# Optimization experiments

Hardware: AMD Instinct MI355X
Metric: run time of the kernel (lower is better)

The kernel has to match this reference:

```python
import jax, jax.numpy as jnp
import numpy as np

B, T, DIM, H = 4, 2048, 1024, 16
NOPE, ROPE, VDIM, KVR = 128, 64, 128, 512
QKD = NOPE + ROPE  # 192
SCALE = QKD ** -0.5
THETA = 10000.0


def apply_rope(x, cos, sin):
    # x: (B, T, H, D) with interleaved (real, imag) pairs; cos/sin: (T, D//2)
    xr, xi = x[..., 0::2], x[..., 1::2]
    c = cos[None, :, None, :]
    s = sin[None, :, None, :]
    yr = xr * c - xi * s
    yi = xr * s + xi * c
    return jnp.stack([yr, yi], axis=-1).reshape(x.shape)


def rms_norm(x, eps=1e-6):
    return x * jax.lax.rsqrt(jnp.mean(x * x, axis=-1, keepdims=True) + eps)


def setup_inputs() -> dict:
    key = jax.random.key(0)
    ks = jax.random.split(key, 10)
    def lin(k, fan_in, fan_out):
        bound = 1.0 / np.sqrt(fan_in)
        kw, kb = jax.random.split(k)
        w = jax.random.uniform(kw, (fan_out, fan_in), jnp.float32, -bound, bound)
        b = jax.random.uniform(kb, (fan_out,), jnp.float32, -bound, bound)
        return w, b
    wq_w, wq_b = lin(ks[0], DIM, H * QKD)
    wkv_a_w, wkv_a_b = lin(ks[1], DIM, KVR + ROPE)
    wkv_b_w, wkv_b_b = lin(ks[2], KVR, H * (NOPE + VDIM))
    wo_w, wo_b = lin(ks[3], H * VDIM, DIM)
    x = jax.random.normal(ks[4], (B, T, DIM), jnp.float32)
    inv_freq = THETA ** (-jnp.arange(0, ROPE, 2, dtype=jnp.float32) / ROPE)  # (32,)
    ang = jnp.arange(T, dtype=jnp.float32)[:, None] * inv_freq[None, :]  # (T, 32)
    return {
        "x": x,
        "wq_w": wq_w, "wq_b": wq_b,
        "wkv_a_w": wkv_a_w, "wkv_a_b": wkv_a_b,
        "wkv_b_w": wkv_b_w, "wkv_b_b": wkv_b_b,
        "wo_w": wo_w, "wo_b": wo_b,
        "freqs_cos": jnp.cos(ang), "freqs_sin": jnp.sin(ang),
        "start_pos": 0,
    }


def reference(x, wq_w, wq_b, wkv_a_w, wkv_a_b, wkv_b_w, wkv_b_b, wo_w, wo_b,
              freqs_cos, freqs_sin, start_pos):
    b, t, _ = x.shape
    # Q projection, split into nope + rope parts
    q = (x @ wq_w.T + wq_b).reshape(b, t, H, QKD)
    q_nope, q_rope = q[..., :NOPE], q[..., NOPE:]
    q_rope = apply_rope(q_rope, freqs_cos, freqs_sin)
    q = jnp.concatenate([q_nope, q_rope], axis=-1)  # (B,T,H,192)
    # low-rank KV latent + shared rope key
    kv_a = x @ wkv_a_w.T + wkv_a_b  # (B,T,576)
    kv_lat, k_rope = kv_a[..., :KVR], kv_a[..., KVR:]
    k_rope = apply_rope(k_rope[:, :, None, :], freqs_cos, freqs_sin)  # (B,T,1,64)
    # decompress latent -> k_nope, v
    kv = (rms_norm(kv_lat) @ wkv_b_w.T + wkv_b_b).reshape(b, t, H, NOPE + VDIM)
    k_nope, v = kv[..., :NOPE], kv[..., NOPE:]
    k = jnp.concatenate([k_nope, jnp.broadcast_to(k_rope, (b, t, H, ROPE))], axis=-1)
    # causal SDPA (start_pos=0 prefill: cache[:end_pos] == current k/v)
    scores = jnp.einsum("bthd,bshd->bhts", q, k) * SCALE
    causal = jnp.tril(jnp.ones((t, t), dtype=bool))
    scores = jnp.where(causal[None, None], scores, jnp.finfo(scores.dtype).min)
    probs = jax.nn.softmax(scores, axis=-1)
    out = jnp.einsum("bhts,bshd->bthd", probs, v).reshape(b, t, H * VDIM)
    return out @ wo_w.T + wo_b
```

## Files before the change

### kernel.cpp

```cpp
#include <hip/hip_runtime.h>
#include <hip/hip_bf16.h>
#include <cmath>

#define B_    4
#define T_    2048
#define DIM_  1024
#define H_    16
#define NOPE_ 128
#define ROPE_ 64
#define VDIM_ 128
#define KVR_  512
#define QKD_  192
#define NTOK  (B_ * T_)

static constexpr float SCALE2_ = 0.07216878364870322f * 1.4426950408889634f;

typedef __attribute__((ext_vector_type(8))) unsigned short ushort8_t;
typedef __bf16 v8bf __attribute__((ext_vector_type(8)));
typedef float  v4f  __attribute__((ext_vector_type(4)));

__device__ __forceinline__ float bf2f(unsigned short u) {
    return __uint_as_float(((unsigned int)u) << 16);
}
__device__ __forceinline__ unsigned short f2bf(float f) {
    unsigned int u = __float_as_uint(f);
    u += 0x7FFFu + ((u >> 16) & 1u);
    return (unsigned short)(u >> 16);
}
__device__ __forceinline__ unsigned short f2bf_hw(float f) {
    return __builtin_bit_cast(unsigned short, (__bf16)f);
}
__device__ __forceinline__ void store1(float* p, float v)          { *p = v; }
__device__ __forceinline__ void store1(__hip_bfloat16* p, float v) { *p = __float2bfloat16(v); }

__device__ __forceinline__ float exp2_hw(float x) {
    return __builtin_amdgcn_exp2f(x);
}

__device__ __forceinline__ void load_lds16(const void* g, void* l) {
    __builtin_amdgcn_global_load_lds(
        (const __attribute__((address_space(1))) void*)g,
        (__attribute__((address_space(3))) void*)l, 16, 0, 0);
}

__device__ __forceinline__ void cvt4(const float* s, __hip_bfloat16* d, int q4) {
    const int i = q4 * 4;
    const float4 v = *(const float4*)(s + i);
    ushort4 o;
    o.x = f2bf(v.x); o.y = f2bf(v.y); o.z = f2bf(v.z); o.w = f2bf(v.w);
    *(ushort4*)((unsigned short*)d + i) = o;
}

#define X4_   (NTOK*1024/4)
#define Q4_   (3072*1024/4)
#define KB4_  (4096*512/4)
#define O4_   (1024*2048/4)
#define A4_   (640*1024/4)
#define CVT_TOTAL (X4_ + Q4_ + KB4_ + O4_ + A4_)

__global__ __launch_bounds__(256) void cvt_all(
    const float* __restrict__ x,    const float* __restrict__ wq,
    const float* __restrict__ wkvb, const float* __restrict__ wo,
    const float* __restrict__ wkva, const float* __restrict__ wkva_bias,
    __hip_bfloat16* __restrict__ xb,    __hip_bfloat16* __restrict__ wqb,
    __hip_bfloat16* __restrict__ wkvbb, __hip_bfloat16* __restrict__ wob,
    __hip_bfloat16* __restrict__ wkvab, float* __restrict__ bias_pad)
{
    int idx = blockIdx.x * 256 + threadIdx.x;
    if (idx < X4_) { cvt4(x, xb, idx); return; }
    idx -= X4_;
    if (idx < Q4_) { cvt4(wq, wqb, idx); return; }
    idx -= Q4_;
    if (idx < KB4_) { cvt4(wkvb, wkvbb, idx); return; }
    idx -= KB4_;
    if (idx < O4_) { cvt4(wo, wob, idx); return; }
    idx -= O4_;
    if (idx < A4_) {
        const int i = idx * 4;
        ushort4 o;
        if (i < 576 * 1024) {
            const float4 v = *(const float4*)(wkva + i);
            o.x = f2bf(v.x); o.y = f2bf(v.y); o.z = f2bf(v.z); o.w = f2bf(v.w);
        } else {
            o.x = o.y = o.z = o.w = 0;
        }
        *(ushort4*)((unsigned short*)wkvab + i) = o;
        if (idx < 640) bias_pad[idx] = (idx < 576) ? wkva_bias[idx] : 0.0f;
    }
}

template <typename CT, int EPI>
__global__ __launch_bounds__(256) void gemm_mfma(
    const __hip_bfloat16* __restrict__ A, int lda,
    const __hip_bfloat16* __restrict__ W, int ldw,
    const float* __restrict__ bias,
    CT* __restrict__ C, int ldc, int K,
    unsigned short* __restrict__ kvf)
{
    __shared__ unsigned short smem[2 * 128 * 32];
    unsigned short* A_s = smem;
    unsigned short* B_s = smem + 128 * 32;

    const int tid  = threadIdx.x;
    const int ln   = tid & 63;
    const int wv   = tid >> 6;
    const int l15  = ln & 15;
    const int quad = ln >> 4;
    const int wm   = wv & 1, wn = wv >> 1;
    const int n0 = blockIdx.x * 128, m0 = blockIdx.y * 128;

    v4f acc[4][4] = {};

    for (int k0 = 0; k0 < K; k0 += 32) {
        __syncthreads();
        #pragma unroll
        for (int it = 0; it < 2; ++it) {
            const int idx = it * 256 + wv * 64;
            const int li  = idx + ln;
            const int row = li >> 2, ch = li & 3;
            load_lds16(A + (size_t)(m0 + row) * lda + k0 + ch * 8, &A_s[idx * 8]);
            load_lds16(W + (size_t)(n0 + row) * ldw + k0 + ch * 8, &B_s[idx * 8]);
        }
        __syncthreads();

        v8bf af[4], bf_[4];
        #pragma unroll
        for (int i = 0; i < 4; ++i) {
            af[i]  = *(const v8bf*)&A_s[(wm * 64 + i * 16 + l15) * 32 + quad * 8];
            bf_[i] = *(const v8bf*)&B_s[(wn * 64 + i * 16 + l15) * 32 + quad * 8];
        }
        #pragma unroll
        for (int i = 0; i < 4; ++i)
            #pragma unroll
            for (int j = 0; j < 4; ++j)
                acc[i][j] = __builtin_amdgcn_mfma_f32_16x16x32_bf16(
                                af[i], bf_[j], acc[i][j], 0, 0, 0);
    }

    if (EPI == 0) {
        #pragma unroll
        for (int i = 0; i < 4; ++i) {
            const int mrow = m0 + wm * 64 + i * 16 + quad * 4;
            #pragma unroll
            for (int j = 0; j < 4; ++j) {
                const int ncol = n0 + wn * 64 + j * 16 + l15;
                const float bb = bias[ncol];
                #pragma unroll
                for (int r = 0; r < 4; ++r)
                    store1(C + (size_t)(mrow + r) * ldc + ncol, acc[i][j][r] + bb);
            }
        }
    } else {
        const int head = n0 >> 8;
        const bool is_v = (n0 & 128) != 0;
        __syncthreads();
        #pragma unroll
        for (int p = 0; p < 2; ++p) {
            if (p) __syncthreads();
            if (wm == p) {
                #pragma unroll
                for (int i = 0; i < 4; ++i) {
                    #pragma unroll
                    for (int j = 0; j < 4; ++j) {
                        const int ncl = wn * 64 + j * 16 + l15;
                        const float bb = bias[n0 + ncl];
                        #pragma unroll
                        for (int r = 0; r < 4; ++r) {
                            const unsigned short v = f2bf(acc[i][j][r] + bb);
                            const int lnf = quad * 4 + r;
                            int off;
                            if (!is_v) {
                                const int s = ncl >> 5, qf = (ncl >> 3) & 3, e = ncl & 7;
                                off = (s * 4 + i) * 512 + (qf * 16 + lnf) * 8 + e;
                            } else {
                                const int nt = ncl >> 4, lnv = ncl & 15;
                                const int jj = i * 16 + lnf;
                                const int s2 = jj >> 5, qv = (jj >> 3) & 3, ev = jj & 7;
                                off = (nt * 2 + s2) * 512 + (qv * 16 + lnv) * 8 + ev;
                            }
                            smem[off] = v;
                        }
                    }
                }
            }
            __syncthreads();
            const size_t GT = (size_t)(m0 >> 6) + p;
            unsigned short* dst = kvf + ((GT * 16 + head) << 14) + (is_v ? 16 * 512 : 0);
            #pragma unroll
            for (int it = 0; it < 4; ++it) {
                const int u = (tid + it * 256) * 8;
                *(ushort8_t*)(dst + u) = *(const ushort8_t*)&smem[u];
            }
        }
    }
}

__global__ __launch_bounds__(256) void gemm_qkva(
    const __hip_bfloat16* __restrict__ A,
    const __hip_bfloat16* __restrict__ Wq, const float* __restrict__ biasq,
    __hip_bfloat16* __restrict__ Cq,
    const __hip_bfloat16* __restrict__ Wa, const float* __restrict__ biasa,
    __hip_bfloat16* __restrict__ Ca)
{
    __shared__ unsigned short smem[2 * 128 * 32];
    unsigned short* A_s = smem;
    unsigned short* B_s = smem + 128 * 32;

    const bool is_q = blockIdx.x < 24;
    const __hip_bfloat16* W = is_q ? Wq : Wa;
    const float* bias       = is_q ? biasq : biasa;
    __hip_bfloat16* C       = is_q ? Cq : Ca;
    const int ldc = is_q ? 3072 : 640;
    const int n0  = (is_q ? blockIdx.x : (blockIdx.x - 24)) * 128;
    const int m0  = blockIdx.y * 128;

    const int tid  = threadIdx.x;
    const int ln   = tid & 63;
    const int wv   = tid >> 6;
    const int l15  = ln & 15;
    const int quad = ln >> 4;
    const int wm   = wv & 1, wn = wv >> 1;

    v4f acc[4][4] = {};

    for (int k0 = 0; k0 < 1024; k0 += 32) {
        __syncthreads();
        #pragma unroll
        for (int it = 0; it < 2; ++it) {
            const int idx = it * 256 + wv * 64;
            const int li  = idx + ln;
            const int row = li >> 2, ch = li & 3;
            load_lds16(A + (size_t)(m0 + row) * 1024 + k0 + ch * 8, &A_s[idx * 8]);
            load_lds16(W + (size_t)(n0 + row) * 1024 + k0 + ch * 8, &B_s[idx * 8]);
        }
        __syncthreads();

        v8bf af[4], bf_[4];
        #pragma unroll
        for (int i = 0; i < 4; ++i) {
            af[i]  = *(const v8bf*)&A_s[(wm * 64 + i * 16 + l15) * 32 + quad * 8];
            bf_[i] = *(const v8bf*)&B_s[(wn * 64 + i * 16 + l15) * 32 + quad * 8];
        }
        #pragma unroll
        for (int i = 0; i < 4; ++i)
            #pragma unroll
            for (int j = 0; j < 4; ++j)
                acc[i][j] = __builtin_amdgcn_mfma_f32_16x16x32_bf16(
                                af[i], bf_[j], acc[i][j], 0, 0, 0);
    }

    #pragma unroll
    for (int i = 0; i < 4; ++i) {
        const int mrow = m0 + wm * 64 + i * 16 + quad * 4;
        #pragma unroll
        for (int j = 0; j < 4; ++j) {
            const int ncol = n0 + wn * 64 + j * 16 + l15;
            const float bb = bias[ncol];
            #pragma unroll
            for (int r = 0; r < 4; ++r)
                C[(size_t)(mrow + r) * ldc + ncol] = __float2bfloat16(acc[i][j][r] + bb);
        }
    }
}

__global__ __launch_bounds__(256) void rmsnorm_ropek(
    const __hip_bfloat16* __restrict__ kva,
    __hip_bfloat16* __restrict__ kvn,
    __hip_bfloat16* __restrict__ kr,
    const float* __restrict__ cs,
    const float* __restrict__ sn)
{
    const int tok = blockIdx.x;
    const int tid = threadIdx.x;
    const __hip_bfloat16* row = kva + (size_t)tok * 640;

    const float x0 = __bfloat162float(row[tid]);
    const float x1 = __bfloat162float(row[tid + 256]);
    float ss = x0*x0 + x1*x1;
    #pragma unroll
    for (int off = 32; off >= 1; off >>= 1)
        ss += __shfl_down(ss, off);

    __shared__ float red[4];
    __shared__ float scale_sh;
    if ((tid & 63) == 0) red[tid >> 6] = ss;
    __syncthreads();
    if (tid == 0) {
        const float tot = red[0] + red[1] + red[2] + red[3];
        scale_sh = rsqrtf(tot * (1.0f/512.0f) + 1e-6f);
    }
    __syncthreads();
    const float sc = scale_sh;
    kvn[(size_t)tok*512 + tid]       = __float2bfloat16(x0 * sc);
    kvn[(size_t)tok*512 + tid + 256] = __float2bfloat16(x1 * sc);

    if (tid < 32) {
        const int t = tok & (T_ - 1);
        const float c = cs[t*32 + tid];
        const float s = sn[t*32 + tid];
        const float xr = __bfloat162float(row[KVR_ + 2*tid]);
        const float xi = __bfloat162float(row[KVR_ + 2*tid + 1]);
        kr[(size_t)tok*64 + 2*tid]     = __float2bfloat16(xr * c - xi * s);
        kr[(size_t)tok*64 + 2*tid + 1] = __float2bfloat16(xr * s + xi * c);
    }
}

__device__ __forceinline__ void attn_stage_regs(
    v8bf* R,
    const unsigned short* __restrict__ kvf,
    const __hip_bfloat16* __restrict__ kr,
    size_t tokb, int j0, int h, int wv, int lane, int tid)
{
    const size_t GT = (tokb + j0) >> 6;
    const unsigned short* base = kvf + ((GT * 16 + h) << 14);
    #pragma unroll
    for (int i = 0; i < 4; ++i)
        R[i] = *(const v8bf*)(base + ((wv * 4 + i) << 9) + lane * 8);
    const int j = tid >> 3, dch = tid & 7;
    R[4] = *(const v8bf*)((const unsigned short*)kr + (tokb + j0 + j) * 64 + dch * 8);
}

__global__ __launch_bounds__(512, 2) void attn_mfma(
    const __hip_bfloat16* __restrict__ q,
    const unsigned short* __restrict__ kvf,
    const __hip_bfloat16* __restrict__ kr,
    const float* __restrict__ cs,
    const float* __restrict__ sn,
    __hip_bfloat16* __restrict__ att)
{
    __shared__ unsigned short KVf[40 * 512];
    __shared__ unsigned short P_s[8][2][16 * 72];

    const int tid  = threadIdx.x;
    const int lane = tid & 63;
    const int ln   = tid & 15;
    const int quad = (tid >> 4) & 3;
    const int wv   = tid >> 6;

    const int bid  = (int)(blockIdx.x + 8u * blockIdx.y + 128u * blockIdx.z);
    const int half = bid >> 8;
    const int id2  = bid & 255;
    const int pr   = id2 & 3;
    const int h    = (id2 >> 2) & 15;
    const int b    = id2 >> 6;
    const int qt   = half ? pr : (7 - pr);

    const int q0 = qt * 256;
    const size_t tokb = (size_t)b * T_;

    v8bf qf[2][6];
    #pragma unroll
    for (int st = 0; st < 2; ++st) {
        const int trow = q0 + st*128 + wv*16 + ln;
        const __hip_bfloat16* qrow =
            q + (tokb + trow) * (size_t)(H_*QKD_) + h*QKD_;
        #pragma unroll
        for (int s = 0; s < 6; ++s) {
            ushort8_t raw = *(const ushort8_t*)(qrow + s*32 + quad*8);
            ushort8_t o;
            if (s < 4) {
                #pragma unroll
                for (int i = 0; i < 8; ++i)
                    o[i] = f2bf(bf2f(raw[i]) * SCALE2_);
            } else {
                #pragma unroll
                for (int p2 = 0; p2 < 4; ++p2) {
                    const int fi = (s-4)*16 + quad*4 + p2;
                    const float c  = cs[trow*32 + fi];
                    const float sv = sn[trow*32 + fi];
                    const float xr = bf2f(raw[p2*2]);
                    const float xi = bf2f(raw[p2*2+1]);
                    o[p2*2]   = f2bf((xr*c - xi*sv) * SCALE2_);
                    o[p2*2+1] = f2bf((xr*sv + xi*c) * SCALE2_);
                }
            }
            qf[st][s] = __builtin_bit_cast(v8bf, o);
        }
    }

    v4f O[2][8];
    #pragma unroll
    for (int st = 0; st < 2; ++st)
        #pragma unroll
        for (int nt = 0; nt < 8; ++nt) O[st][nt] = (v4f){0.f, 0.f, 0.f, 0.f};
    float m_r[2][4], l_r[2][4];
    #pragma unroll
    for (int st = 0; st < 2; ++st)
        #pragma unroll
        for (int r = 0; r < 4; ++r) { m_r[st][r] = -1e30f; l_r[st][r] = 0.0f; }

    const int qmin0 = q0 + wv*16;
    const int qmin1 = q0 + 128 + wv*16;
    const int nkt = (q0 + 256) >> 6;

    const int slot0 = (wv < 4) ? (wv * 4) : (wv * 4 + 8);
    const int krj = tid >> 3, krd = tid & 7;
    const int krfrag = 16 + (krd >> 2) * 4 + (krj >> 4);
    const int kroff  = krfrag * 512 + ((krd & 3) * 16 + (krj & 15)) * 8;

    v8bf R[5];
    attn_stage_regs(R, kvf, kr, tokb, 0, h, wv, lane, tid);

    for (int kt = 0; kt < nkt; ++kt) {
        const int j0 = kt << 6;

        #pragma unroll
        for (int i = 0; i < 4; ++i)
            *(v8bf*)&KVf[(slot0 + i) * 512 + lane * 8] = R[i];
        *(v8bf*)&KVf[kroff] = R[4];
        __syncthreads();

        if (kt + 1 < nkt)
            attn_stage_regs(R, kvf, kr, tokb, j0 + 64, h, wv, lane, tid);

        const bool act0 = (j0 <= qmin0 + 15);
        const bool act1 = (j0 <= qmin1 + 15);

        if (act1) {
            v4f S[2][4];
            #pragma unroll
            for (int st = 0; st < 2; ++st)
                #pragma unroll
                for (int t = 0; t < 4; ++t) S[st][t] = (v4f){0.f, 0.f, 0.f, 0.f};
            __builtin_amdgcn_s_setprio(1);
            if (act0) {
                #pragma unroll
                for (int s = 0; s < 6; ++s)
                    #pragma unroll
                    for (int t = 0; t < 4; ++t) {
                        const v8bf kb = *(const v8bf*)&KVf[(s*4 + t)*512 + lane*8];
                        S[0][t] = __builtin_amdgcn_mfma_f32_16x16x32_bf16(qf[0][s], kb, S[0][t], 0, 0, 0);
                        S[1][t] = __builtin_amdgcn_mfma_f32_16x16x32_bf16(qf[1][s], kb, S[1][t], 0, 0, 0);
                    }
            } else {
                #pragma unroll
                for (int s = 0; s < 6; ++s)
                    #pragma unroll
                    for (int t = 0; t < 4; ++t) {
                        const v8bf kb = *(const v8bf*)&KVf[(s*4 + t)*512 + lane*8];
                        S[1][t] = __builtin_amdgcn_mfma_f32_16x16x32_bf16(qf[1][s], kb, S[1][t], 0, 0, 0);
                    }
            }
            __builtin_amdgcn_s_setprio(0);

            #pragma unroll
            for (int st = 0; st < 2; ++st) {
                if (st == 0 && !act0) continue;
                const int qmin = (st == 0) ? qmin0 : qmin1;
                if (j0 + 63 > qmin) {
                    #pragma unroll
                    for (int t = 0; t < 4; ++t) {
                        const int kpos = j0 + t*16 + ln;
                        #pragma unroll
                        for (int r = 0; r < 4; ++r)
                            if (kpos > qmin + quad*4 + r) S[st][t][r] = -1e30f;
                    }
                }
                float mx[4];
                bool need = false;
                #pragma unroll
                for (int r = 0; r < 4; ++r) {
                    float m2 = fmaxf(fmaxf(S[st][0][r], S[st][1][r]),
                                     fmaxf(S[st][2][r], S[st][3][r]));
                    #pragma unroll
                    for (int off = 1; off < 16; off <<= 1)
                        m2 = fmaxf(m2, __shfl_xor(m2, off));
                    mx[r] = m2;
                    need = need || (m2 > m_r[st][r] + 8.0f);
                }
                if (__any((int)need)) {
                    #pragma unroll
                    for (int r = 0; r < 4; ++r) {
                        const float mn = fmaxf(m_r[st][r], mx[r]);
                        const float alpha = exp2_hw(m_r[st][r] - mn);
                        m_r[st][r] = mn;
                        l_r[st][r] *= alpha;
                        #pragma unroll
                        for (int nt = 0; nt < 8; ++nt)
                            O[st][nt][r] *= alpha;
                    }
                }
                float rs[4] = {0.f, 0.f, 0.f, 0.f};
                #pragma unroll
                for (int t = 0; t < 4; ++t)
                    #pragma unroll
                    for (int r = 0; r < 4; ++r) {
                        const float pp = exp2_hw(S[st][t][r] - m_r[st][r]);
                        S[st][t][r] = pp;
                        rs[r] += pp;
                    }
                #pragma unroll
                for (int r = 0; r < 4; ++r) {
                    #pragma unroll
                    for (int off = 1; off < 16; off <<= 1)
                        rs[r] += __shfl_xor(rs[r], off);
                    l_r[st][r] += rs[r];
                }
                #pragma unroll
                for (int t = 0; t < 4; ++t)
                    #pragma unroll
                    for (int r = 0; r < 4; ++r)
                        P_s[wv][st][(quad*4 + r)*72 + t*16 + ln] = f2bf_hw(S[st][t][r]);
            }

            __builtin_amdgcn_s_setprio(1);
            #pragma unroll
            for (int s2 = 0; s2 < 2; ++s2) {
                const v8bf pa1 = *(const v8bf*)&P_s[wv][1][ln*72 + s2*32 + quad*8];
                if (act0) {
                    const v8bf pa0 = *(const v8bf*)&P_s[wv][0][ln*72 + s2*32 + quad*8];
                    #pragma unroll
                    for (int nt = 0; nt < 8; ++nt) {
                        const v8bf vb = *(const v8bf*)&KVf[(24 + nt*2 + s2)*512 + lane*8];
                        O[0][nt] = __builtin_amdgcn_mfma_f32_16x16x32_bf16(pa0, vb, O[0][nt], 0, 0, 0);
                        O[1][nt] = __builtin_amdgcn_mfma_f32_16x16x32_bf16(pa1, vb, O[1][nt], 0, 0, 0);
                    }
                } else {
                    #pragma unroll
                    for (int nt = 0; nt < 8; ++nt) {
                        const v8bf vb = *(const v8bf*)&KVf[(24 + nt*2 + s2)*512 + lane*8];
                        O[1][nt] = __builtin_amdgcn_mfma_f32_16x16x32_bf16(pa1, vb, O[1][nt], 0, 0, 0);
                    }
                }
            }
            __builtin_amdgcn_s_setprio(0);
        }
        __syncthreads();
    }

    #pragma unroll
    for (int st = 0; st < 2; ++st) {
        __hip_bfloat16* obase =
            att + (tokb + q0 + st*128 + wv*16) * (size_t)(H_*VDIM_) + h*VDIM_;
        #pragma unroll
        for (int r = 0; r < 4; ++r) {
            const float inv = 1.0f / l_r[st][r];
            __hip_bfloat16* orow = obase + (size_t)(quad*4 + r) * (H_*VDIM_);
            #pragma unroll
            for (int nt = 0; nt < 8; ++nt)
                orow[nt*16 + ln] = __float2bfloat16(O[st][nt][r] * inv);
        }
    }
}

__global__ void fill_zero(float* p, int n) {
    int i = blockIdx.x * 256 + threadIdx.x;
    if (i < n) p[i] = 0.0f;
}

extern "C" void kernel_launch(void* const* d_in, const int* in_sizes, int n_in,
                              void* d_out, int out_size, void* d_ws, size_t ws_size,
                              hipStream_t stream)
{
    const float* x      = (const float*)d_in[0];
    const float* wq_w   = (const float*)d_in[1];
    const float* wq_b   = (const float*)d_in[2];
    const float* wkva_w = (const float*)d_in[3];
    const float* wkva_b = (const float*)d_in[4];
    const float* wkvb_w = (const float*)d_in[5];
    const float* wkvb_b = (const float*)d_in[6];
    const float* wo_w   = (const float*)d_in[7];
    const float* wo_b   = (const float*)d_in[8];
    const float* cs     = (const float*)d_in[9];
    const float* sn     = (const float*)d_in[10];

    const size_t q_b    = (size_t)NTOK * 3072 * 2;
    const size_t kvf_b  = (size_t)128 * 16 * 32 * 512 * 2;
    const size_t xb_b   = (size_t)NTOK * 1024 * 2;
    const size_t kvap_b = (size_t)NTOK * 640 * 2;
    const size_t kvn_b  = (size_t)NTOK * 512 * 2;
    const size_t wq_b_b = (size_t)3072 * 1024 * 2;
    const size_t wkva_b_b = (size_t)640 * 1024 * 2;
    const size_t wkvb_b_b = (size_t)4096 * 512 * 2;
    const size_t wo_b_b   = (size_t)1024 * 2048 * 2;
    const size_t bias_b   = 4096;
    const size_t need = q_b + kvf_b + xb_b + kvap_b + kvn_b +
                        wq_b_b + wkva_b_b + wkvb_b_b + wo_b_b + bias_b;

    if (ws_size < need) {
        fill_zero<<<(out_size + 255) / 256, 256, 0, stream>>>((float*)d_out, out_size);
        return;
    }

    char* p = (char*)d_ws;
    __hip_bfloat16* q    = (__hip_bfloat16*)p;             p += q_b;
    unsigned short* kvf  = (unsigned short*)p;             p += kvf_b;
    char*           dynr = p;
    __hip_bfloat16* xb   = (__hip_bfloat16*)p;             p += xb_b;
    __hip_bfloat16* kvap = (__hip_bfloat16*)p;             p += kvap_b;
    __hip_bfloat16* kvn  = (__hip_bfloat16*)p;             p += kvn_b;
    __hip_bfloat16* wq_bf = (__hip_bfloat16*)p;
    __hip_bfloat16* kr    = (__hip_bfloat16*)p;            p += wq_b_b;
    __hip_bfloat16* wkva_bf = (__hip_bfloat16*)p;          p += wkva_b_b;
    __hip_bfloat16* wkvb_bf = (__hip_bfloat16*)p;          p += wkvb_b_b;
    __hip_bfloat16* wo_bf   = (__hip_bfloat16*)p;          p += wo_b_b;
    float*          bias_pad = (float*)p;
    __hip_bfloat16* attb = (__hip_bfloat16*)dynr;
    float*          out  = (float*)d_out;

    cvt_all<<<CVT_TOTAL / 256, 256, 0, stream>>>(
        x, wq_w, wkvb_w, wo_w, wkva_w, wkva_b,
        xb, wq_bf, wkvb_bf, wo_bf, wkva_bf, bias_pad);

    gemm_qkva<<<dim3(29, NTOK/128), 256, 0, stream>>>(
        xb, wq_bf, wq_b, q, wkva_bf, bias_pad, kvap);

    rmsnorm_ropek<<<NTOK, 256, 0, stream>>>(kvap, kvn, kr, cs, sn);

    gemm_mfma<__hip_bfloat16, 1><<<dim3(4096/128, NTOK/128), 256, 0, stream>>>(
        kvn, 512, wkvb_bf, 512, wkvb_b, (( __hip_bfloat16*)nullptr), 0, 512, kvf);

    attn_mfma<<<dim3(T_/256, H_, B_), 512, 0, stream>>>(q, kvf, kr, cs, sn, attb);

    gemm_mfma<float, 0><<<dim3(1024/128, NTOK/128), 256, 0, stream>>>(
        attb, 2048, wo_bf, 2048, wo_b, out, 1024, 2048, nullptr);
}
```

Baseline: 528.2 us.

## Transpose attention MFMAs to keep P in registers and drop LDS round-trip

Swaps the MFMA operand order so the score and output tiles hold a query row per lane column. The softmax max and sum reductions then need only two cross-lane shuffles per stage instead of a per-row 16-lane reduction, and the running max and sum shrink to one scalar per stage. The P matrix is packed to bf16 with v_cvt_pk_bf16 and rearranged into the PV A-operand layout through lane shuffles, which removes the per-wave LDS scratch buffer and its write/read round trip. The launch bound is raised to 4 blocks per CU, and outputs are written as packed 32-bit stores. The extra shuffles and the tighter register budget could cause spills or lower MFMA throughput.

```diff
diff --git a/kernel.cpp b/kernel.cpp
--- a/kernel.cpp
+++ b/kernel.cpp
@@ -18,6 +18,7 @@
 typedef __attribute__((ext_vector_type(8))) unsigned short ushort8_t;
 typedef __bf16 v8bf __attribute__((ext_vector_type(8)));
 typedef float  v4f  __attribute__((ext_vector_type(4)));
+typedef unsigned int v4u __attribute__((ext_vector_type(4)));
 
 __device__ __forceinline__ float bf2f(unsigned short u) {
     return __uint_as_float(((unsigned int)u) << 16);
@@ -29,6 +30,11 @@
 }
 __device__ __forceinline__ unsigned short f2bf_hw(float f) {
     return __builtin_bit_cast(unsigned short, (__bf16)f);
+}
+__device__ __forceinline__ unsigned int cvt_pk_bf16(float lo, float hi) {
+    unsigned int r;
+    asm("v_cvt_pk_bf16_f32 %0, %1, %2" : "=v"(r) : "v"(lo), "v"(hi));
+    return r;
 }
 __device__ __forceinline__ void store1(float* p, float v)          { *p = v; }
 __device__ __forceinline__ void store1(__hip_bfloat16* p, float v) { *p = __float2bfloat16(v); }
@@ -320,7 +326,7 @@
     R[4] = *(const v8bf*)((const unsigned short*)kr + (tokb + j0 + j) * 64 + dch * 8);
 }
 
-__global__ __launch_bounds__(512, 2) void attn_mfma(
+__global__ __launch_bounds__(512, 4) void attn_mfma(
     const __hip_bfloat16* __restrict__ q,
     const unsigned short* __restrict__ kvf,
     const __hip_bfloat16* __restrict__ kr,
@@ -329,13 +335,14 @@
     __hip_bfloat16* __restrict__ att)
 {
     __shared__ unsigned short KVf[40 * 512];
-    __shared__ unsigned short P_s[8][2][16 * 72];
 
     const int tid  = threadIdx.x;
     const int lane = tid & 63;
     const int ln   = tid & 15;
     const int quad = (tid >> 4) & 3;
     const int wv   = tid >> 6;
+    const int hf   = quad >> 1;
+    const int p2   = quad & 1;
 
     const int bid  = (int)(blockIdx.x + 8u * blockIdx.y + 128u * blockIdx.z);
     const int half = bid >> 8;
@@ -361,17 +368,17 @@
             if (s < 4) {
                 #pragma unroll
                 for (int i = 0; i < 8; ++i)
-                    o[i] = f2bf(bf2f(raw[i]) * SCALE2_);
+                    o[i] = f2bf_hw(bf2f(raw[i]) * SCALE2_);
             } else {
                 #pragma unroll
-                for (int p2 = 0; p2 < 4; ++p2) {
-                    const int fi = (s-4)*16 + quad*4 + p2;
+                for (int pp2 = 0; pp2 < 4; ++pp2) {
+                    const int fi = (s-4)*16 + quad*4 + pp2;
                     const float c  = cs[trow*32 + fi];
                     const float sv = sn[trow*32 + fi];
-                    const float xr = bf2f(raw[p2*2]);
-                    const float xi = bf2f(raw[p2*2+1]);
-                    o[p2*2]   = f2bf((xr*c - xi*sv) * SCALE2_);
-                    o[p2*2+1] = f2bf((xr*sv + xi*c) * SCALE2_);
+                    const float xr = bf2f(raw[pp2*2]);
+                    const float xi = bf2f(raw[pp2*2+1]);
+                    o[pp2*2]   = f2bf_hw((xr*c - xi*sv) * SCALE2_);
+                    o[pp2*2+1] = f2bf_hw((xr*sv + xi*c) * SCALE2_);
                 }
             }
             qf[st][s] = __builtin_bit_cast(v8bf, o);
@@ -383,11 +390,8 @@
     for (int st = 0; st < 2; ++st)
         #pragma unroll
         for (int nt = 0; nt < 8; ++nt) O[st][nt] = (v4f){0.f, 0.f, 0.f, 0.f};
-    float m_r[2][4], l_r[2][4];
-    #pragma unroll
-    for (int st = 0; st < 2; ++st)
-        #pragma unroll
-        for (int r = 0; r < 4; ++r) { m_r[st][r] = -1e30f; l_r[st][r] = 0.0f; }
+    float m_r[2] = {-1e30f, -1e30f};
+    float l_r[2] = {0.0f, 0.0f};
 
     const int qmin0 = q0 + wv*16;
     const int qmin1 = q0 + 128 + wv*16;
@@ -429,8 +433,8 @@
                     #pragma unroll
                     for (int t = 0; t < 4; ++t) {
                         const v8bf kb = *(const v8bf*)&KVf[(s*4 + t)*512 + lane*8];
-                        S[0][t] = __builtin_amdgcn_mfma_f32_16x16x32_bf16(qf[0][s], kb, S[0][t], 0, 0, 0);
-                        S[1][t] = __builtin_amdgcn_mfma_f32_16x16x32_bf16(qf[1][s], kb, S[1][t], 0, 0, 0);
+                        S[0][t] = __builtin_amdgcn_mfma_f32_16x16x32_bf16(kb, qf[0][s], S[0][t], 0, 0, 0);
+                        S[1][t] = __builtin_amdgcn_mfma_f32_16x16x32_bf16(kb, qf[1][s], S[1][t], 0, 0, 0);
                     }
             } else {
                 #pragma unroll
@@ -438,90 +442,100 @@
                     #pragma unroll
                     for (int t = 0; t < 4; ++t) {
                         const v8bf kb = *(const v8bf*)&KVf[(s*4 + t)*512 + lane*8];
-                        S[1][t] = __builtin_amdgcn_mfma_f32_16x16x32_bf16(qf[1][s], kb, S[1][t], 0, 0, 0);
+                        S[1][t] = __builtin_amdgcn_mfma_f32_16x16x32_bf16(kb, qf[1][s], S[1][t], 0, 0, 0);
                     }
             }
             __builtin_amdgcn_s_setprio(0);
 
+            v8bf pfrag[2][2];
             #pragma unroll
             for (int st = 0; st < 2; ++st) {
                 if (st == 0 && !act0) continue;
                 const int qmin = (st == 0) ? qmin0 : qmin1;
+                const int qrow = qmin + ln;
                 if (j0 + 63 > qmin) {
                     #pragma unroll
                     for (int t = 0; t < 4; ++t) {
-                        const int kpos = j0 + t*16 + ln;
+                        const int kbase = j0 + t*16 + quad*4;
                         #pragma unroll
                         for (int r = 0; r < 4; ++r)
-                            if (kpos > qmin + quad*4 + r) S[st][t][r] = -1e30f;
+                            if (kbase + r > qrow) S[st][t][r] = -1e30f;
                     }
                 }
-                float mx[4];
-                bool need = false;
-                #pragma unroll
-                for (int r = 0; r < 4; ++r) {
-                    float m2 = fmaxf(fmaxf(S[st][0][r], S[st][1][r]),
-                                     fmaxf(S[st][2][r], S[st][3][r]));
-                    #pragma unroll
-                    for (int off = 1; off < 16; off <<= 1)
-                        m2 = fmaxf(m2, __shfl_xor(m2, off));
-                    mx[r] = m2;
-                    need = need || (m2 > m_r[st][r] + 8.0f);
+                float mx = S[st][0][0];
+                #pragma unroll
+                for (int t = 0; t < 4; ++t)
+                    #pragma unroll
+                    for (int r = 0; r < 4; ++r)
+                        if (t || r) mx = fmaxf(mx, S[st][t][r]);
+                mx = fmaxf(mx, __shfl_xor(mx, 16));
+                mx = fmaxf(mx, __shfl_xor(mx, 32));
+                const bool need = mx > m_r[st] + 8.0f;
+                if (__any((int)need)) {
+                    const float mn = fmaxf(m_r[st], mx);
+                    const float alpha = exp2_hw(m_r[st] - mn);
+                    m_r[st] = mn;
+                    l_r[st] *= alpha;
+                    #pragma unroll
+                    for (int nt = 0; nt < 8; ++nt)
+                        O[st][nt] *= alpha;
                 }
-                if (__any((int)need)) {
+                float rs = 0.0f;
+                #pragma unroll
+                for (int t = 0; t < 4; ++t)
                     #pragma unroll
                     for (int r = 0; r < 4; ++r) {
-                        const float mn = fmaxf(m_r[st][r], mx[r]);
-                        const float alpha = exp2_hw(m_r[st][r] - mn);
-                        m_r[st][r] = mn;
-                        l_r[st][r] *= alpha;
-                        #pragma unroll
-                        for (int nt = 0; nt < 8; ++nt)
-                            O[st][nt][r] *= alpha;
+                        const float pp = exp2_hw(S[st][t][r] - m_r[st]);
+                        S[st][t][r] = pp;
+                        rs += pp;
+                    }
+                rs += __shfl_xor(rs, 16);
+                rs += __shfl_xor(rs, 32);
+                l_r[st] += rs;
+                unsigned int pk[4][2];
+                #pragma unroll
+                for (int t = 0; t < 4; ++t)
+                    #pragma unroll
+                    for (int i = 0; i < 2; ++i)
+                        pk[t][i] = cvt_pk_bf16(S[st][t][2*i], S[st][t][2*i+1]);
+                #pragma unroll
+                for (int s2 = 0; s2 < 2; ++s2) {
+                    const unsigned int A0 = pk[2*s2][0],   A1 = pk[2*s2][1];
+                    const unsigned int B0 = pk[2*s2+1][0], B1 = pk[2*s2+1][1];
+                    const unsigned int sB0 = __shfl_xor(B0, 32), sB1 = __shfl_xor(B1, 32);
+                    const unsigned int sA0 = __shfl_xor(A0, 32), sA1 = __shfl_xor(A1, 32);
+                    const unsigned int U0 = hf ? sB0 : A0;
+                    const unsigned int U1 = hf ? sB1 : A1;
+                    const unsigned int V0 = hf ? B0 : sA0;
+                    const unsigned int V1 = hf ? B1 : sA1;
+                    const unsigned int xU0 = __shfl_xor(U0, 16), xU1 = __shfl_xor(U1, 16);
+                    const unsigned int xV0 = __shfl_xor(V0, 16), xV1 = __shfl_xor(V1, 16);
+                    v4u w;
+                    w.x = p2 ? xV0 : U0;
+                    w.y = p2 ? xV1 : U1;
+                    w.z = p2 ? V0 : xU0;
+                    w.w = p2 ? V1 : xU1;
+                    pfrag[st][s2] = __builtin_bit_cast(v8bf, w);
+                }
+            }
+
+            __builtin_amdgcn_s_setprio(1);
+            #pragma unroll
+            for (int s2 = 0; s2 < 2; ++s2) {
+                if (act0) {
+                    #pragma unroll
+                    for (int nt = 0; nt < 8; ++nt) {
+                        const v8bf vb = *(const v8bf*)&KVf[(24 + nt*2 + s2)*512 + lane*8];
+                        O[0][nt] = __builtin_amdgcn_mfma_f32_16x16x32_bf16(vb, pfrag[0][s2], O[0][nt], 0, 0, 0);
+                        O[1][nt] = __builtin_amdgcn_mfma_f32_16x16x32_bf16(vb, pfrag[1][s2], O[1][nt], 0, 0, 0);
+                    }
+                } else {
+                    #pragma unroll
+                    for (int nt = 0; nt < 8; ++nt) {
+                        const v8bf vb = *(const v8bf*)&KVf[(24 + nt*2 + s2)*512 + lane*8];
+                        O[1][nt] = __builtin_amdgcn_mfma_f32_16x16x32_bf16(vb, pfrag[1][s2], O[1][nt], 0, 0, 0);
                     }
                 }
-                float rs[4] = {0.f, 0.f, 0.f, 0.f};
-                #pragma unroll
-                for (int t = 0; t < 4; ++t)
-                    #pragma unroll
-                    for (int r = 0; r < 4; ++r) {
-                        const float pp = exp2_hw(S[st][t][r] - m_r[st][r]);
-                        S[st][t][r] = pp;
-                        rs[r] += pp;
-                    }
-                #pragma unroll
-                for (int r = 0; r < 4; ++r) {
-                    #pragma unroll
-                    for (int off = 1; off < 16; off <<= 1)
-                        rs[r] += __shfl_xor(rs[r], off);
-                    l_r[st][r] += rs[r];
-                }
-                #pragma unroll
-                for (int t = 0; t < 4; ++t)
-                    #pragma unroll
-                    for (int r = 0; r < 4; ++r)
-                        P_s[wv][st][(quad*4 + r)*72 + t*16 + ln] = f2bf_hw(S[st][t][r]);
-            }
-
-            __builtin_amdgcn_s_setprio(1);
-            #pragma unroll
-            for (int s2 = 0; s2 < 2; ++s2) {
-                const v8bf pa1 = *(const v8bf*)&P_s[wv][1][ln*72 + s2*32 + quad*8];
-                if (act0) {
-                    const v8bf pa0 = *(const v8bf*)&P_s[wv][0][ln*72 + s2*32 + quad*8];
-                    #pragma unroll
-                    for (int nt = 0; nt < 8; ++nt) {
-                        const v8bf vb = *(const v8bf*)&KVf[(24 + nt*2 + s2)*512 + lane*8];
-                        O[0][nt] = __builtin_amdgcn_mfma_f32_16x16x32_bf16(pa0, vb, O[0][nt], 0, 0, 0);
-                        O[1][nt] = __builtin_amdgcn_mfma_f32_16x16x32_bf16(pa1, vb, O[1][nt], 0, 0, 0);
-                    }
-                } else {
-                    #pragma unroll
-                    for (int nt = 0; nt < 8; ++nt) {
-                        const v8bf vb = *(const v8bf*)&KVf[(24 + nt*2 + s2)*512 + lane*8];
-                        O[1][nt] = __builtin_amdgcn_mfma_f32_16x16x32_bf16(pa1, vb, O[1][nt], 0, 0, 0);
-                    }
-                }
             }
             __builtin_amdgcn_s_setprio(0);
         }
@@ -530,15 +544,18 @@
 
     #pragma unroll
     for (int st = 0; st < 2; ++st) {
-        __hip_bfloat16* obase =
-            att + (tokb + q0 + st*128 + wv*16) * (size_t)(H_*VDIM_) + h*VDIM_;
-        #pragma unroll
-        for (int r = 0; r < 4; ++r) {
-            const float inv = 1.0f / l_r[st][r];
-            __hip_bfloat16* orow = obase + (size_t)(quad*4 + r) * (H_*VDIM_);
-            #pragma unroll
-            for (int nt = 0; nt < 8; ++nt)
-                orow[nt*16 + ln] = __float2bfloat16(O[st][nt][r] * inv);
+        const int qrow = q0 + st*128 + wv*16 + ln;
+        const float inv = 1.0f / l_r[st];
+        unsigned short* orow =
+            (unsigned short*)att + (tokb + qrow) * (size_t)(H_*VDIM_) + h*VDIM_;
+        #pragma unroll
+        for (int nt = 0; nt < 8; ++nt) {
+            #pragma unroll
+            for (int rp = 0; rp < 2; ++rp) {
+                const unsigned int w =
+                    cvt_pk_bf16(O[st][nt][2*rp] * inv, O[st][nt][2*rp+1] * inv);
+                *(unsigned int*)(orow + nt*16 + quad*4 + rp*2) = w;
+            }
         }
     }
 }
```

After: 854.5 us. 1.62x slower.
